# Kernel optimization log

Measured on AMD Instinct MI355X. Metric: run time of the kernel, lower is better.

## Reference

```python
import jax, jax.numpy as jnp
import numpy as np

DEPTH = 11  # tree depth -> depth+1 routing steps, n_nodes = 2**(DEPTH+1)-1 = 4095


def setup_inputs() -> dict:
    key = jax.random.key(0)
    k1, k2, k3 = jax.random.split(key, 3)
    B, D_in, D_out = 8192, 2048, 2048
    n_nodes = 2 ** (DEPTH + 1) - 1
    x = jax.random.normal(k1, (B, D_in), dtype=jnp.float32)
    # nn.Linear(input_width, n_nodes, bias=False).weight : (n_nodes, D_in)
    W_in = jax.random.normal(k2, (n_nodes, D_in), dtype=jnp.float32) / np.sqrt(D_in).astype(np.float32)
    # nn.Linear(n_nodes, output_width, bias=False).weight : (D_out, n_nodes)
    W_out = jax.random.normal(k3, (D_out, n_nodes), dtype=jnp.float32) / np.sqrt(n_nodes).astype(np.float32)
    return {"x": x, "W_in": W_in, "W_out": W_out}


def reference(x, W_in, W_out):
    B = x.shape[0]
    # Torch loop recomputes linear_in(x) every step; the result is identical each
    # iteration, so compute the (B, n_nodes) logits once and gather per depth step.
    logits_all = x @ W_in.T  # (B, n_nodes)

    def step(cur, _):
        # gather the logit of each sample's current tree node
        score = jnp.take_along_axis(logits_all, cur[:, None], axis=1)[:, 0]  # (B,)
        nxt = cur * 2 + (score >= 0).astype(jnp.int32) + 1  # left/right child
        return nxt, (cur, score)

    init = jnp.zeros((B,), dtype=jnp.int32)
    _, (nodes, scores) = jax.lax.scan(step, init, None, length=DEPTH + 1)
    nodes = nodes.T    # (B, depth+1) visited node ids
    scores = scores.T  # (B, depth+1) selected logits

    mlp1 = jax.nn.gelu(scores, approximate=False)  # exact GELU, matches nn.GELU
    # Conditional output projection: only the depth+1 visited columns of W_out
    # contribute per sample (FFF / conditional-MoE semantics).
    W_sel = W_out.T[nodes]  # (B, depth+1, D_out)
    return jnp.einsum('bd,bdo->bo', mlp1, W_sel)
```

## Files before the change

kernel.cpp:

```cpp
#include <hip/hip_runtime.h>
#include <math.h>

#define B_SZ    8192
#define D_IN    2048
#define D_OUT   2048
#define N_NODES 4095
#define STEPS   12
#define N_LEAVES 2048

__global__ __launch_bounds__(256) void transpose_wout(
    const float* __restrict__ W, float* __restrict__ Wt) {
  __shared__ float tile[32][33];
  const int tx = threadIdx.x;
  const int ty = threadIdx.y;
  const int col0 = blockIdx.x * 32;
  const int row0 = blockIdx.y * 32;

  #pragma unroll
  for (int i = ty; i < 32; i += 8) {
    const int c = col0 + tx;
    float v = 0.0f;
    if (c < N_NODES) v = W[(size_t)(row0 + i) * N_NODES + c];
    tile[i][tx] = v;
  }
  __syncthreads();
  #pragma unroll
  for (int i = ty; i < 32; i += 8) {
    const int r = col0 + i;
    if (r < N_NODES) Wt[(size_t)r * D_OUT + row0 + tx] = tile[tx][i];
  }
}

__global__ __launch_bounds__(256) void route_kernel(
    const float* __restrict__ x, const float* __restrict__ W_in,
    int* __restrict__ leafArr, float* __restrict__ gsc) {
  const int wave = (int)((blockIdx.x * (size_t)blockDim.x + threadIdx.x) >> 6);
  const int lane = threadIdx.x & 63;
  if (wave >= B_SZ) return;

  const float4* xr = (const float4*)(x + (size_t)wave * D_IN);
  float4 xv[8];
  #pragma unroll
  for (int i = 0; i < 8; ++i) xv[i] = xr[lane + i * 64];

  int cur = 0;
  #pragma unroll
  for (int d = 0; d < STEPS; ++d) {
    const float4* wr = (const float4*)(W_in + (size_t)cur * D_IN);
    float s = 0.0f;
    #pragma unroll
    for (int i = 0; i < 8; ++i) {
      const float4 w = wr[lane + i * 64];
      s += xv[i].x * w.x + xv[i].y * w.y + xv[i].z * w.z + xv[i].w * w.w;
    }
    #pragma unroll
    for (int off = 32; off > 0; off >>= 1) s += __shfl_xor(s, off);

    if (lane == 0) {
      gsc[wave * STEPS + d] = 0.5f * s * (1.0f + erff(s * 0.70710678118654752f));
      if (d == STEPS - 1) leafArr[wave] = cur - 2047;
    }
    cur = cur * 2 + ((s >= 0.0f) ? 2 : 1);
  }
}

__global__ __launch_bounds__(256) void out_kernel(
    const float* __restrict__ Wt, const int* __restrict__ leafArr,
    const float* __restrict__ gsc, float* __restrict__ out) {
  __shared__ int list[B_SZ];
  __shared__ int cnt;
  const int l = blockIdx.x;
  const int t = threadIdx.x;

  if (t == 0) cnt = 0;
  __syncthreads();
  for (int b = t; b < B_SZ; b += 256)
    if (leafArr[b] == l) list[atomicAdd(&cnt, 1)] = b;
  __syncthreads();
  const int n = cnt;
  if (n == 0) return;

  int path[STEPS];
  {
    int nd = l + 2047;
    #pragma unroll
    for (int d = STEPS - 1; d >= 0; --d) { path[d] = nd; nd = (nd - 1) >> 1; }
  }

  #pragma unroll
  for (int c = 0; c < 2; ++c) {
    const int col = c * 1024 + t * 4;
    float4 w[STEPS];
    #pragma unroll
    for (int d = 0; d < STEPS; ++d)
      w[d] = *(const float4*)(Wt + (size_t)path[d] * D_OUT + col);

    for (int s = 0; s < n; ++s) {
      const int b = list[s];
      const float* g = gsc + (size_t)b * STEPS;
      float4 acc = make_float4(0.f, 0.f, 0.f, 0.f);
      #pragma unroll
      for (int d = 0; d < STEPS; ++d) {
        const float gd = g[d];
        acc.x += gd * w[d].x; acc.y += gd * w[d].y;
        acc.z += gd * w[d].z; acc.w += gd * w[d].w;
      }
      *(float4*)(out + (size_t)b * D_OUT + col) = acc;
    }
  }
}

extern "C" void kernel_launch(void* const* d_in, const int* in_sizes, int n_in,
                              void* d_out, int out_size, void* d_ws, size_t ws_size,
                              hipStream_t stream) {
  const float* x     = (const float*)d_in[0];
  const float* W_in  = (const float*)d_in[1];
  const float* W_out = (const float*)d_in[2];
  float* out = (float*)d_out;

  float* Wt      = (float*)d_ws;
  int*   leafArr = (int*)((char*)d_ws + (size_t)N_NODES * D_OUT * sizeof(float));
  float* gsc     = (float*)((char*)leafArr + (size_t)B_SZ * sizeof(int));

  {
    dim3 blk(32, 8);
    dim3 grd((N_NODES + 31) / 32, D_OUT / 32);
    transpose_wout<<<grd, blk, 0, stream>>>(W_out, Wt);
  }
  {
    dim3 blk(256);
    dim3 grd(B_SZ / 4);
    route_kernel<<<grd, blk, 0, stream>>>(x, W_in, leafArr, gsc);
  }
  {
    dim3 blk(256);
    dim3 grd(N_LEAVES);
    out_kernel<<<grd, blk, 0, stream>>>(Wt, leafArr, gsc, out);
  }
}
```

Baseline: 247.7 us.

## Fuse transpose and routing into one launch; group output blocks by depth-10 subtree

Merges the W_out transpose and the routing kernel into one launch, with block index selecting the role, so one kernel launch and the serial gap between them go away and the two independent phases can overlap. The transpose now uses 64x64 tiles with float4 global loads and stores. The output kernel assigns one block per 4-leaf subtree (512 blocks) instead of one per leaf, which cuts the redundant scans of the 8192-entry leaf array and shares the ancestor weight loads across four leaves. This uses more registers per thread and a per-sample select for the last two levels, and it gives fewer blocks with more samples each, which can lower occupancy and load balance.

```diff
diff --git a/kernel.cpp b/kernel.cpp
--- a/kernel.cpp
+++ b/kernel.cpp
@@ -1,41 +1,62 @@
 #include <hip/hip_runtime.h>
 #include <math.h>
 
-#define B_SZ    8192
-#define D_IN    2048
-#define D_OUT   2048
-#define N_NODES 4095
-#define STEPS   12
+#define B_SZ     8192
+#define D_IN     2048
+#define D_OUT    2048
+#define N_NODES  4095
+#define STEPS    12
 #define N_LEAVES 2048
+#define N_SUB    512
 
-__global__ __launch_bounds__(256) void transpose_wout(
-    const float* __restrict__ W, float* __restrict__ Wt) {
-  __shared__ float tile[32][33];
-  const int tx = threadIdx.x;
-  const int ty = threadIdx.y;
-  const int col0 = blockIdx.x * 32;
-  const int row0 = blockIdx.y * 32;
+#define T_BLOCKS 2048
+#define R_BLOCKS 2048
 
-  #pragma unroll
-  for (int i = ty; i < 32; i += 8) {
-    const int c = col0 + tx;
-    float v = 0.0f;
-    if (c < N_NODES) v = W[(size_t)(row0 + i) * N_NODES + c];
-    tile[i][tx] = v;
-  }
-  __syncthreads();
-  #pragma unroll
-  for (int i = ty; i < 32; i += 8) {
-    const int r = col0 + i;
-    if (r < N_NODES) Wt[(size_t)r * D_OUT + row0 + tx] = tile[tx][i];
-  }
-}
-
-__global__ __launch_bounds__(256) void route_kernel(
+__global__ __launch_bounds__(256) void fused_pre(
+    const float* __restrict__ W_out, float* __restrict__ Wt,
     const float* __restrict__ x, const float* __restrict__ W_in,
     int* __restrict__ leafArr, float* __restrict__ gsc) {
-  const int wave = (int)((blockIdx.x * (size_t)blockDim.x + threadIdx.x) >> 6);
-  const int lane = threadIdx.x & 63;
+  __shared__ float tile[64][65];
+  const int bx = blockIdx.x;
+  const int tid = threadIdx.x;
+
+  if (bx < T_BLOCKS) {
+    const int col0 = (bx & 63) * 64;
+    const int row0 = (bx >> 6) * 64;
+    const int r  = tid >> 4;
+    const int c4 = (tid & 15) * 4;
+
+    #pragma unroll
+    for (int i = 0; i < 4; ++i) {
+      const int row = r + i * 16;
+      const float* src = W_out + (size_t)(row0 + row) * N_NODES + col0 + c4;
+      if (col0 + c4 + 3 < N_NODES) {
+        const float4 v = *(const float4*)src;
+        tile[c4 + 0][row] = v.x; tile[c4 + 1][row] = v.y;
+        tile[c4 + 2][row] = v.z; tile[c4 + 3][row] = v.w;
+      } else {
+        #pragma unroll
+        for (int k = 0; k < 4; ++k)
+          tile[c4 + k][row] = (col0 + c4 + k < N_NODES) ? src[k] : 0.0f;
+      }
+    }
+    __syncthreads();
+    #pragma unroll
+    for (int i = 0; i < 4; ++i) {
+      const int rn = r + i * 16;
+      const int node = col0 + rn;
+      if (node < N_NODES) {
+        float4 v;
+        v.x = tile[rn][c4 + 0]; v.y = tile[rn][c4 + 1];
+        v.z = tile[rn][c4 + 2]; v.w = tile[rn][c4 + 3];
+        *(float4*)(Wt + (size_t)node * D_OUT + row0 + c4) = v;
+      }
+    }
+    return;
+  }
+
+  const int wave = (int)(((size_t)(bx - T_BLOCKS) * 256 + tid) >> 6);
+  const int lane = tid & 63;
   if (wave >= B_SZ) return;
 
   const float4* xr = (const float4*)(x + (size_t)wave * D_IN);
@@ -69,41 +90,63 @@
     const float* __restrict__ gsc, float* __restrict__ out) {
   __shared__ int list[B_SZ];
   __shared__ int cnt;
-  const int l = blockIdx.x;
+  const int sub = blockIdx.x;
   const int t = threadIdx.x;
 
   if (t == 0) cnt = 0;
   __syncthreads();
-  for (int b = t; b < B_SZ; b += 256)
-    if (leafArr[b] == l) list[atomicAdd(&cnt, 1)] = b;
+  for (int b = t; b < B_SZ; b += 256) {
+    const int l = leafArr[b];
+    if ((l >> 2) == sub) list[atomicAdd(&cnt, 1)] = (b << 2) | (l & 3);
+  }
   __syncthreads();
   const int n = cnt;
   if (n == 0) return;
 
-  int path[STEPS];
+  int anc[10];
   {
-    int nd = l + 2047;
+    int nd = 511 + sub;
     #pragma unroll
-    for (int d = STEPS - 1; d >= 0; --d) { path[d] = nd; nd = (nd - 1) >> 1; }
+    for (int d = 9; d >= 0; --d) { anc[d] = nd; nd = (nd - 1) >> 1; }
   }
+  const int p10a = 1023 + 2 * sub, p10b = 1024 + 2 * sub;
+  const int leaf0 = 2047 + 4 * sub;
 
   #pragma unroll
   for (int c = 0; c < 2; ++c) {
     const int col = c * 1024 + t * 4;
-    float4 w[STEPS];
+    float4 wa[10], wpA, wpB, wl0, wl1, wl2, wl3;
     #pragma unroll
-    for (int d = 0; d < STEPS; ++d)
-      w[d] = *(const float4*)(Wt + (size_t)path[d] * D_OUT + col);
+    for (int d = 0; d < 10; ++d)
+      wa[d] = *(const float4*)(Wt + (size_t)anc[d] * D_OUT + col);
+    wpA = *(const float4*)(Wt + (size_t)p10a * D_OUT + col);
+    wpB = *(const float4*)(Wt + (size_t)p10b * D_OUT + col);
+    wl0 = *(const float4*)(Wt + (size_t)(leaf0 + 0) * D_OUT + col);
+    wl1 = *(const float4*)(Wt + (size_t)(leaf0 + 1) * D_OUT + col);
+    wl2 = *(const float4*)(Wt + (size_t)(leaf0 + 2) * D_OUT + col);
+    wl3 = *(const float4*)(Wt + (size_t)(leaf0 + 3) * D_OUT + col);
 
     for (int s = 0; s < n; ++s) {
-      const int b = list[s];
+      const int e = list[s];
+      const int b = e >> 2, local = e & 3;
       const float* g = gsc + (size_t)b * STEPS;
       float4 acc = make_float4(0.f, 0.f, 0.f, 0.f);
       #pragma unroll
-      for (int d = 0; d < STEPS; ++d) {
+      for (int d = 0; d < 10; ++d) {
         const float gd = g[d];
-        acc.x += gd * w[d].x; acc.y += gd * w[d].y;
-        acc.z += gd * w[d].z; acc.w += gd * w[d].w;
+        acc.x += gd * wa[d].x; acc.y += gd * wa[d].y;
+        acc.z += gd * wa[d].z; acc.w += gd * wa[d].w;
+      }
+      {
+        const float gd = g[10];
+        const float4 w = (local & 2) ? wpB : wpA;
+        acc.x += gd * w.x; acc.y += gd * w.y; acc.z += gd * w.z; acc.w += gd * w.w;
+      }
+      {
+        const float gd = g[11];
+        const float4 w = (local & 2) ? ((local & 1) ? wl3 : wl2)
+                                     : ((local & 1) ? wl1 : wl0);
+        acc.x += gd * w.x; acc.y += gd * w.y; acc.z += gd * w.z; acc.w += gd * w.w;
       }
       *(float4*)(out + (size_t)b * D_OUT + col) = acc;
     }
@@ -122,19 +165,8 @@
   int*   leafArr = (int*)((char*)d_ws + (size_t)N_NODES * D_OUT * sizeof(float));
   float* gsc     = (float*)((char*)leafArr + (size_t)B_SZ * sizeof(int));
 
-  {
-    dim3 blk(32, 8);
-    dim3 grd((N_NODES + 31) / 32, D_OUT / 32);
-    transpose_wout<<<grd, blk, 0, stream>>>(W_out, Wt);
-  }
-  {
-    dim3 blk(256);
-    dim3 grd(B_SZ / 4);
-    route_kernel<<<grd, blk, 0, stream>>>(x, W_in, leafArr, gsc);
-  }
-  {
-    dim3 blk(256);
-    dim3 grd(N_LEAVES);
-    out_kernel<<<grd, blk, 0, stream>>>(Wt, leafArr, gsc, out);
-  }
+  fused_pre<<<dim3(T_BLOCKS + R_BLOCKS), dim3(256), 0, stream>>>(
+      W_out, Wt, x, W_in, leafArr, gsc);
+
+  out_kernel<<<dim3(N_SUB), dim3(256), 0, stream>>>(Wt, leafArr, gsc, out);
 }
```

After: 274.6 us. 1.11x slower.
